# Kernel tuning notes

Hardware: AMD Instinct MI355X
Metric: run time of the kernel (lower is better)

Reference implementation:

```python
import jax, jax.numpy as jnp
import numpy as np

B, S, D, H, RANK, NC = 2, 2048, 1024, 16, 128, 16
DH = D // H


def setup_inputs() -> dict:
    key = jax.random.key(0)
    ks = jax.random.split(key, 10)
    x = jax.random.normal(ks[0], (B, S, D), jnp.float32)
    # causal mask, broadcast over batch and heads like torch's [B,1,S,S]
    mask = jnp.tril(jnp.ones((S, S), dtype=bool))[None, None]
    # orthogonal-ish init approximated by scaled gaussian
    compress_neurons = jax.random.normal(ks[1], (NC, D, RANK), jnp.float32) / np.sqrt(D)
    router_Q = jax.random.normal(ks[2], (NC, D), jnp.float32) * 0.02
    router_K = jax.random.normal(ks[3], (NC, D), jnp.float32) * 0.02
    router_V = jax.random.normal(ks[4], (NC, D), jnp.float32) * 0.02
    wQ = jax.random.normal(ks[5], (D, RANK), jnp.float32) / np.sqrt(RANK)
    wK = jax.random.normal(ks[6], (D, RANK), jnp.float32) / np.sqrt(RANK)
    wV = jax.random.normal(ks[7], (D, RANK), jnp.float32) / np.sqrt(RANK)
    wO = jax.random.normal(ks[8], (D, D), jnp.float32) / np.sqrt(D)
    return {"x": x, "mask": mask, "compress_neurons": compress_neurons,
            "router_Q": router_Q, "router_K": router_K, "router_V": router_V,
            "wQ": wQ, "wK": wK, "wV": wV, "wO": wO}


def reference(x, mask, compress_neurons, router_Q, router_K, router_V, wQ, wK, wV, wO):
    def compress(router_w):
        # router scores -> softmax over all n_compress neurons
        w = jax.nn.softmax(jnp.einsum('bsd,nd->bsn', x, router_w), axis=-1)  # [B,S,NC]
        # softmax-weighted sum of all neuron projections (fused einsum)
        return jnp.einsum('bsd,ndr,bsn->bsr', x, compress_neurons, w)  # [B,S,RANK]

    hQ = compress(router_Q)
    hK = compress(router_K)
    hV = compress(router_V)
    # expand rank -> d_model (Linear weight [D,RANK]), then split heads
    Q = jnp.einsum('bsr,dr->bsd', hQ, wQ).reshape(B, S, H, DH).transpose(0, 2, 1, 3)
    K = jnp.einsum('bsr,dr->bsd', hK, wK).reshape(B, S, H, DH).transpose(0, 2, 1, 3)
    V = jnp.einsum('bsr,dr->bsd', hV, wV).reshape(B, S, H, DH).transpose(0, 2, 1, 3)
    scores = jnp.einsum('bhqd,bhkd->bhqk', Q, K) / np.sqrt(DH)  # [B,H,S,S]
    scores = jnp.where(mask, scores, -jnp.inf)
    attn = jax.nn.softmax(scores, axis=-1)
    attn_out = jnp.einsum('bhqk,bhkd->bhqd', attn, V)
    attn_out = attn_out.transpose(0, 2, 1, 3).reshape(B, S, D)
    # dropout omitted (eval mode / dropout=0)
    return jnp.einsum('bsd,ed->bse', attn_out, wO)
```

## Files before the change

kernel.cpp:

```cpp
#include <hip/hip_runtime.h>
#include <hip/hip_bf16.h>
#include <math.h>

#define B_ 2
#define S_ 2048
#define D_ 1024
#define H_ 16
#define RANK_ 128
#define NC_ 16
#define DH_ 64
#define T_ (B_*S_)
#define NZ_ 2176

typedef __attribute__((ext_vector_type(8))) __bf16 bf16x8;
typedef __attribute__((ext_vector_type(8))) unsigned short u16x8;
typedef __attribute__((ext_vector_type(4))) float f32x4;

#if __has_builtin(__builtin_amdgcn_exp2f)
#define EXP2F(x) __builtin_amdgcn_exp2f(x)
#else
#define EXP2F(x) exp2f(x)
#endif

__device__ __forceinline__ unsigned short f2bu(float f) {
    __hip_bfloat16 h = __float2bfloat16(f);
    unsigned short u; __builtin_memcpy(&u, &h, 2); return u;
}
__device__ __forceinline__ float bu2f(unsigned short u) {
    __hip_bfloat16 h; __builtin_memcpy(&h, &u, 2); return __bfloat162float(h);
}

__device__ __forceinline__ void gl_lds16(const unsigned short* g, unsigned short* l) {
    __builtin_amdgcn_global_load_lds(
        (const __attribute__((address_space(1))) void*)g,
        (__attribute__((address_space(3))) void*)l, 16, 0, 0);
}

__device__ __forceinline__ bool sniff_f32(const unsigned* __restrict__ p) {
    int votes = 0;
    #pragma unroll
    for (int i = 0; i < 64; i++) {
        unsigned e = (p[i] >> 23) & 0xFFu;
        votes += (e >= 0x60u && e <= 0x8Fu) ? 1 : 0;
    }
    return votes >= 32;
}

struct Cvt { const void* src[9]; unsigned short* dst[9]; const void* C; unsigned short* Ct; };

__global__ __launch_bounds__(256) void k_inputs(Cvt cv,
    const unsigned* __restrict__ probe)
{
    bool f32 = sniff_f32(probe);
    if (blockIdx.x < 512) {
        int bid = blockIdx.x;
        int d0 = (bid & 15) * 64, r0 = ((bid >> 4) & 1) * 64, n = bid >> 5;
        __shared__ unsigned short tile[64][65];
        for (int idx = threadIdx.x; idx < 4096; idx += 256) {
            int row = idx >> 6, col = idx & 63;
            size_t si = ((size_t)n*D_ + d0 + row)*RANK_ + r0 + col;
            tile[row][col] = f32 ? f2bu(((const float*)cv.C)[si])
                                 : ((const unsigned short*)cv.C)[si];
        }
        __syncthreads();
        for (int idx = threadIdx.x; idx < 4096; idx += 256) {
            int row = idx >> 6, col = idx & 63;
            cv.Ct[((size_t)(n*RANK_ + r0 + row))*D_ + d0 + col] = tile[col][row];
        }
        return;
    }
    const int offs[9] = {0, 4194304, 4210688, 4227072, 4243456,
                         4259840, 4390912, 4521984, 4653056};
    const int total = 5701632;
    int nconv = gridDim.x - 512;
    int stride = nconv * 256;
    for (int i = (blockIdx.x - 512) * 256 + threadIdx.x; i < total; i += stride) {
        int seg = 0;
        #pragma unroll
        for (int s = 1; s < 9; s++) seg += (i >= offs[s]) ? 1 : 0;
        int local = i - offs[seg];
        const void* sp = cv.src[seg];
        unsigned short v = 0;
        if (sp) v = f32 ? f2bu(((const float*)sp)[local]) : ((const unsigned short*)sp)[local];
        cv.dst[seg][local] = v;
    }
}

__global__ __launch_bounds__(256) void k_transposeV(const unsigned short* __restrict__ V,
    unsigned short* __restrict__ Vtg)
{
    int t0 = blockIdx.x * 64, hcol = blockIdx.y;
    __shared__ unsigned short tile[64][65];
    for (int idx = threadIdx.x; idx < 4096; idx += 256) {
        int row = idx >> 6, col = idx & 63;
        tile[row][col] = V[(size_t)(t0 + row)*D_ + hcol*64 + col];
    }
    __syncthreads();
    int bb = t0 >> 11, s0 = t0 & 2047;
    for (int idx = threadIdx.x; idx < 4096; idx += 256) {
        int dh = idx >> 6, col = idx & 63;
        Vtg[(size_t)((bb*H_ + hcol)*64 + dh)*S_ + s0 + col] = tile[col][dh];
    }
}

template<int MT, int MODE>
__global__ __launch_bounds__(256) void k_mfma_gemm(const unsigned short* __restrict__ A0,
    const unsigned short* __restrict__ Bm, void* __restrict__ Cout,
    const unsigned* __restrict__ probe, int M, int N, int K)
{
    bool f32out = false;
    if (MODE == 2) f32out = sniff_f32(probe);
    __shared__ __align__(16) unsigned short As[MT*32*32];
    __shared__ __align__(16) unsigned short Bs[128*32];
    const int tid = threadIdx.x;
    const int wv = tid >> 6, lane = tid & 63;
    const int wm = (wv >> 1) * (MT*16), wn = (wv & 1) * 64;
    const int quad = lane >> 4, l16 = lane & 15;
    const int m0 = blockIdx.x * (MT*32), n0 = blockIdx.y * 128;

    const unsigned short* A = A0;
    unsigned short* outb = (unsigned short*)Cout;
    int colBase = n0, outStride = N;
    float scale = 1.f;
    if (MODE == 1) {
        int w = n0 >> 10;
        A = A0 + (size_t)w * T_ * RANK_;
        outb = (unsigned short*)Cout + (size_t)w * T_ * D_;
        colBase = n0 & 1023; outStride = D_;
        if (w == 0) scale = 0.125f * 1.44269504f;
    }

    const f32x4 z4 = {0.f, 0.f, 0.f, 0.f};
    f32x4 acc[MT][4];
    #pragma unroll
    for (int i = 0; i < MT; i++)
        #pragma unroll
        for (int j = 0; j < 4; j++) acc[i][j] = z4;

    for (int k0 = 0; k0 < K; k0 += 32) {
        __syncthreads();
        #pragma unroll
        for (int c = 0; c < MT/2; c++) {
            int idx = wv*64 + c*256 + lane;
            gl_lds16(A + (size_t)(m0 + (idx >> 2))*K + k0 + (idx & 3)*8,
                     &As[(wv*64 + c*256)*8]);
        }
        #pragma unroll
        for (int c = 0; c < 2; c++) {
            int idx = wv*64 + c*256 + lane;
            gl_lds16(Bm + (size_t)(n0 + (idx >> 2))*K + k0 + (idx & 3)*8,
                     &Bs[(wv*64 + c*256)*8]);
        }
        __syncthreads();
        bf16x8 af[MT], bfr[4];
        #pragma unroll
        for (int mt = 0; mt < MT; mt++) af[mt]  = *(const bf16x8*)&As[(wm + mt*16 + l16)*32 + quad*8];
        #pragma unroll
        for (int nt = 0; nt < 4; nt++) bfr[nt] = *(const bf16x8*)&Bs[(wn + nt*16 + l16)*32 + quad*8];
        #pragma unroll
        for (int mt = 0; mt < MT; mt++)
            #pragma unroll
            for (int nt = 0; nt < 4; nt++)
                acc[mt][nt] = __builtin_amdgcn_mfma_f32_16x16x32_bf16(af[mt], bfr[nt], acc[mt][nt], 0, 0, 0);
    }
    #pragma unroll
    for (int mt = 0; mt < MT; mt++)
        #pragma unroll
        for (int nt = 0; nt < 4; nt++) {
            int col = colBase + wn + nt*16 + l16;
            #pragma unroll
            for (int r = 0; r < 4; r++) {
                int rowg = m0 + wm + mt*16 + quad*4 + r;
                float v = acc[mt][nt][r] * scale;
                if (MODE == 2 && f32out) ((float*)Cout)[(size_t)rowg*outStride + col] = v;
                else                     outb[(size_t)rowg*outStride + col] = f2bu(v);
            }
        }
}

__global__ __launch_bounds__(256) void k_hreduce(const unsigned short* __restrict__ z,
    unsigned short* __restrict__ h)
{
    int t0 = blockIdx.x * 2;
    int tg = threadIdx.x >> 7, r = threadIdx.x & 127;
    int t = t0 + tg;
    __shared__ float sc[2][48];
    __shared__ float wl[2][3][16];
    if (threadIdx.x < 96) {
        int tk = threadIdx.x / 48, j = threadIdx.x % 48;
        sc[tk][j] = bu2f(z[(size_t)(t0 + tk)*NZ_ + 2048 + j]);
    }
    __syncthreads();
    if (threadIdx.x < 6) {
        int tk = threadIdx.x / 3, w = threadIdx.x % 3;
        float m = -INFINITY;
        for (int n = 0; n < 16; n++) m = fmaxf(m, sc[tk][w*16 + n]);
        float s = 0.f, e[16];
        for (int n = 0; n < 16; n++) { e[n] = __expf(sc[tk][w*16 + n] - m); s += e[n]; }
        float inv = 1.f / s;
        for (int n = 0; n < 16; n++) wl[tk][w][n] = e[n] * inv;
    }
    __syncthreads();
    const unsigned short* zr = z + (size_t)t * NZ_;
    float acc[3] = {0.f, 0.f, 0.f};
    #pragma unroll
    for (int n = 0; n < NC_; n++) {
        float zv = bu2f(zr[n*RANK_ + r]);
        #pragma unroll
        for (int w = 0; w < 3; w++) acc[w] += wl[tg][w][n] * zv;
    }
    #pragma unroll
    for (int w = 0; w < 3; w++) h[((size_t)w*T_ + t)*RANK_ + r] = f2bu(acc[w]);
}

__global__ __launch_bounds__(256) void k_flash_mfma(const unsigned short* __restrict__ Qm,
    const unsigned short* __restrict__ Km, const unsigned short* __restrict__ Vtg,
    unsigned short* __restrict__ Om)
{
    const int p = blockIdx.x, hh = blockIdx.y, b = blockIdx.z;
    __shared__ __align__(16) unsigned short Ks[128*64];
    __shared__ __align__(16) unsigned short Vt[64*128];
    __shared__ __align__(16) unsigned short Ps[64][136];
    const int tid = threadIdx.x;
    const int w = tid >> 6, lane = tid & 63;
    const int quad = lane >> 4, l16 = lane & 15;
    const size_t base  = ((size_t)b * S_) * D_ + (size_t)hh * DH_;
    const size_t vbase = (size_t)((b*H_ + hh) * 64) * S_;
    const f32x4 z4 = {0.f, 0.f, 0.f, 0.f};

    for (int rep = 0; rep < 2; rep++) {
        const int qt = rep ? (31 - p) : p;

        bf16x8 aq[2];
        #pragma unroll
        for (int s = 0; s < 2; s++)
            aq[s] = *(const bf16x8*)(Qm + base + (size_t)(qt*64 + w*16 + l16)*D_ + s*32 + quad*8);

        f32x4 oacc[4];
        #pragma unroll
        for (int nt = 0; nt < 4; nt++) oacc[nt] = z4;
        float lsum[4] = {0.f, 0.f, 0.f, 0.f};

        const int nkt = (qt >> 1) + 1;
        for (int kt = 0; kt < nkt; kt++) {
            __syncthreads();
            #pragma unroll
            for (int c = 0; c < 4; c++) {
                int idx = c*256 + tid;
                int row = idx >> 3, j = (idx & 7) ^ (row & 7);
                gl_lds16(Km + base + (size_t)(kt*128 + row)*D_ + j*8, &Ks[(c*256 + (w<<6))*8]);
            }
            #pragma unroll
            for (int c = 0; c < 4; c++) {
                int idx = c*256 + tid;
                int row = idx >> 4, j = (idx & 15) ^ (row & 7);
                gl_lds16(Vtg + vbase + (size_t)row*S_ + kt*128 + j*8, &Vt[(c*256 + (w<<6))*8]);
            }
            __syncthreads();

            f32x4 sacc[8];
            #pragma unroll
            for (int nt = 0; nt < 8; nt++) sacc[nt] = z4;
            #pragma unroll
            for (int s = 0; s < 2; s++)
                #pragma unroll
                for (int nt = 0; nt < 8; nt++) {
                    int row = nt*16 + l16;
                    int cc = (s*4 + quad) ^ (row & 7);
                    bf16x8 bk = *(const bf16x8*)&Ks[row*64 + cc*8];
                    sacc[nt] = __builtin_amdgcn_mfma_f32_16x16x32_bf16(aq[s], bk, sacc[nt], 0, 0, 0);
                }
            if (kt == (qt >> 1)) {
                #pragma unroll
                for (int nt = 0; nt < 8; nt++) {
                    int key = kt*128 + nt*16 + l16;
                    #pragma unroll
                    for (int r = 0; r < 4; r++)
                        if (key > qt*64 + w*16 + quad*4 + r) sacc[nt][r] = -INFINITY;
                }
            }
            #pragma unroll
            for (int r = 0; r < 4; r++) {
                float rs = 0.f;
                #pragma unroll
                for (int nt = 0; nt < 8; nt++) {
                    float pv = EXP2F(sacc[nt][r]);
                    rs += pv;
                    Ps[w*16 + quad*4 + r][nt*16 + l16] = f2bu(pv);
                }
                lsum[r] += rs;
            }
            #pragma unroll
            for (int s = 0; s < 4; s++) {
                bf16x8 ap = *(const bf16x8*)&Ps[w*16 + l16][s*32 + quad*8];
                #pragma unroll
                for (int nt = 0; nt < 4; nt++) {
                    int row = nt*16 + l16;
                    int cc = (s*4 + quad) ^ (row & 7);
                    bf16x8 bv = *(const bf16x8*)&Vt[row*128 + cc*8];
                    oacc[nt] = __builtin_amdgcn_mfma_f32_16x16x32_bf16(ap, bv, oacc[nt], 0, 0, 0);
                }
            }
        }
        #pragma unroll
        for (int r = 0; r < 4; r++) {
            float l = lsum[r];
            #pragma unroll
            for (int off = 1; off < 16; off <<= 1) l += __shfl_xor(l, off, 64);
            float inv = 1.f / l;
            int tok = qt*64 + w*16 + quad*4 + r;
            #pragma unroll
            for (int nt = 0; nt < 4; nt++)
                Om[base + (size_t)tok*D_ + nt*16 + l16] = f2bu(oacc[nt][r] * inv);
        }
    }
}

extern "C" void kernel_launch(void* const* d_in, const int* in_sizes, int n_in,
                              void* d_out, int out_size, void* d_ws, size_t ws_size,
                              hipStream_t stream)
{
    const unsigned* probe = (const unsigned*)d_in[0];

    unsigned short* u = (unsigned short*)d_ws;
    unsigned short* xc   = u;               size_t o = (size_t)T_*D_;
    unsigned short* wqkv = u + o;           o += (size_t)3*D_*RANK_;
    unsigned short* wOc  = u + o;           o += (size_t)D_*D_;
    unsigned short* Ct   = u + o;           o += (size_t)NZ_*D_;
    unsigned short* h3   = u + o;           o += (size_t)3*T_*RANK_;
    unsigned short* QKVb = u + o;           o += (size_t)3*T_*D_;
    unsigned short* Vtg  = u + o;           o += (size_t)T_*D_;
    unsigned short* z    = u + o;           o += (size_t)T_*NZ_;
    unsigned short* attnb= u + o;           o += (size_t)T_*D_;

    unsigned short* Rp = Ct + (size_t)2048*D_;
    unsigned short* Qb = QKVb;
    unsigned short* Kb = QKVb + (size_t)T_*D_;
    unsigned short* Vb = QKVb + (size_t)2*T_*D_;

    Cvt cv;
    cv.src[0] = d_in[0]; cv.dst[0] = xc;
    cv.src[1] = d_in[3]; cv.dst[1] = Rp;
    cv.src[2] = d_in[4]; cv.dst[2] = Rp + 16384;
    cv.src[3] = d_in[5]; cv.dst[3] = Rp + 32768;
    cv.src[4] = nullptr; cv.dst[4] = Rp + 49152;
    cv.src[5] = d_in[6]; cv.dst[5] = wqkv;
    cv.src[6] = d_in[7]; cv.dst[6] = wqkv + 131072;
    cv.src[7] = d_in[8]; cv.dst[7] = wqkv + 262144;
    cv.src[8] = d_in[9]; cv.dst[8] = wOc;
    cv.C = d_in[2]; cv.Ct = Ct;
    k_inputs<<<512 + 2048, 256, 0, stream>>>(cv, probe);

    k_mfma_gemm<4,0><<<dim3(T_/128, NZ_/128), 256, 0, stream>>>(
        xc, Ct, z, nullptr, T_, NZ_, D_);

    k_hreduce<<<T_/2, 256, 0, stream>>>(z, h3);

    k_mfma_gemm<4,1><<<dim3(T_/128, 3*D_/128), 256, 0, stream>>>(
        h3, wqkv, QKVb, nullptr, T_, 3*D_, RANK_);

    k_transposeV<<<dim3(T_/64, H_), 256, 0, stream>>>(Vb, Vtg);

    k_flash_mfma<<<dim3(16, H_, B_), 256, 0, stream>>>(Qb, Kb, Vtg, attnb);

    k_mfma_gemm<2,2><<<dim3(T_/64, D_/128), 256, 0, stream>>>(
        attnb, wOc, d_out, probe, T_, D_, D_);
}
```

Before: 245.8 us.

## Fuse V transpose into QKV GEMM and double-buffer K tiles in flash attention

A new QKV kernel computes Q and K as before and computes V transposed directly by swapping GEMM operands, which removes the separate transpose kernel and one full write and read of V. The flash attention kernel now double-buffers K tiles in LDS, prefetching the next tile while computing on the current one. V fragments are loaded straight from global memory into registers instead of being staged through LDS. This removes a kernel launch and a sync per iteration, but raises register pressure, and the direct V loads in the flash loop are strided rather than coalesced.

```diff
diff --git a/kernel.cpp b/kernel.cpp
--- a/kernel.cpp
+++ b/kernel.cpp
@@ -86,25 +86,8 @@
     }
 }
 
-__global__ __launch_bounds__(256) void k_transposeV(const unsigned short* __restrict__ V,
-    unsigned short* __restrict__ Vtg)
-{
-    int t0 = blockIdx.x * 64, hcol = blockIdx.y;
-    __shared__ unsigned short tile[64][65];
-    for (int idx = threadIdx.x; idx < 4096; idx += 256) {
-        int row = idx >> 6, col = idx & 63;
-        tile[row][col] = V[(size_t)(t0 + row)*D_ + hcol*64 + col];
-    }
-    __syncthreads();
-    int bb = t0 >> 11, s0 = t0 & 2047;
-    for (int idx = threadIdx.x; idx < 4096; idx += 256) {
-        int dh = idx >> 6, col = idx & 63;
-        Vtg[(size_t)((bb*H_ + hcol)*64 + dh)*S_ + s0 + col] = tile[col][dh];
-    }
-}
-
 template<int MT, int MODE>
-__global__ __launch_bounds__(256) void k_mfma_gemm(const unsigned short* __restrict__ A0,
+__global__ __launch_bounds__(256) void k_mfma_gemm(const unsigned short* __restrict__ A,
     const unsigned short* __restrict__ Bm, void* __restrict__ Cout,
     const unsigned* __restrict__ probe, int M, int N, int K)
 {
@@ -118,18 +101,6 @@
     const int quad = lane >> 4, l16 = lane & 15;
     const int m0 = blockIdx.x * (MT*32), n0 = blockIdx.y * 128;
 
-    const unsigned short* A = A0;
-    unsigned short* outb = (unsigned short*)Cout;
-    int colBase = n0, outStride = N;
-    float scale = 1.f;
-    if (MODE == 1) {
-        int w = n0 >> 10;
-        A = A0 + (size_t)w * T_ * RANK_;
-        outb = (unsigned short*)Cout + (size_t)w * T_ * D_;
-        colBase = n0 & 1023; outStride = D_;
-        if (w == 0) scale = 0.125f * 1.44269504f;
-    }
-
     const f32x4 z4 = {0.f, 0.f, 0.f, 0.f};
     f32x4 acc[MT][4];
     #pragma unroll
@@ -167,13 +138,93 @@
     for (int mt = 0; mt < MT; mt++)
         #pragma unroll
         for (int nt = 0; nt < 4; nt++) {
-            int col = colBase + wn + nt*16 + l16;
+            int col = n0 + wn + nt*16 + l16;
             #pragma unroll
             for (int r = 0; r < 4; r++) {
                 int rowg = m0 + wm + mt*16 + quad*4 + r;
+                float v = acc[mt][nt][r];
+                if (MODE == 2 && f32out) ((float*)Cout)[(size_t)rowg*N + col] = v;
+                else  ((unsigned short*)Cout)[(size_t)rowg*N + col] = f2bu(v);
+            }
+        }
+}
+
+__global__ __launch_bounds__(256) void k_qkv2(const unsigned short* __restrict__ h3,
+    const unsigned short* __restrict__ wqkv, unsigned short* __restrict__ QKb,
+    unsigned short* __restrict__ Vtg)
+{
+    __shared__ __align__(16) unsigned short As[128*32];
+    __shared__ __align__(16) unsigned short Bs[128*32];
+    const int tid = threadIdx.x;
+    const int wv = tid >> 6, lane = tid & 63;
+    const int wm = (wv >> 1) * 64, wn = (wv & 1) * 64;
+    const int quad = lane >> 4, l16 = lane & 15;
+
+    const bool vt = (blockIdx.x >= 512);
+    int m0, n0;
+    const unsigned short *A, *Bm;
+    float scale = 1.f;
+    if (!vt) {
+        int id = blockIdx.x;
+        m0 = (id & 31) * 128;
+        n0 = (id >> 5) * 128;
+        int w = n0 >> 10;
+        A  = h3 + (size_t)w * T_ * RANK_ + (size_t)m0 * RANK_;
+        Bm = wqkv + (size_t)w * D_ * RANK_ + (size_t)(n0 & 1023) * RANK_;
+        if (w == 0) scale = 0.125f * 1.44269504f;
+    } else {
+        int id = blockIdx.x - 512;
+        m0 = (id & 7) * 128;
+        n0 = (id >> 3) * 128;
+        A  = wqkv + (size_t)2 * D_ * RANK_ + (size_t)m0 * RANK_;
+        Bm = h3 + (size_t)2 * T_ * RANK_ + (size_t)n0 * RANK_;
+    }
+
+    const f32x4 z4 = {0.f, 0.f, 0.f, 0.f};
+    f32x4 acc[4][4];
+    #pragma unroll
+    for (int i = 0; i < 4; i++)
+        #pragma unroll
+        for (int j = 0; j < 4; j++) acc[i][j] = z4;
+
+    for (int k0 = 0; k0 < RANK_; k0 += 32) {
+        __syncthreads();
+        #pragma unroll
+        for (int c = 0; c < 2; c++) {
+            int idx = wv*64 + c*256 + lane;
+            gl_lds16(A  + (size_t)(idx >> 2)*RANK_ + k0 + (idx & 3)*8,
+                     &As[(wv*64 + c*256)*8]);
+            gl_lds16(Bm + (size_t)(idx >> 2)*RANK_ + k0 + (idx & 3)*8,
+                     &Bs[(wv*64 + c*256)*8]);
+        }
+        __syncthreads();
+        bf16x8 af[4], bfr[4];
+        #pragma unroll
+        for (int mt = 0; mt < 4; mt++) af[mt]  = *(const bf16x8*)&As[(wm + mt*16 + l16)*32 + quad*8];
+        #pragma unroll
+        for (int nt = 0; nt < 4; nt++) bfr[nt] = *(const bf16x8*)&Bs[(wn + nt*16 + l16)*32 + quad*8];
+        #pragma unroll
+        for (int mt = 0; mt < 4; mt++)
+            #pragma unroll
+            for (int nt = 0; nt < 4; nt++)
+                acc[mt][nt] = __builtin_amdgcn_mfma_f32_16x16x32_bf16(af[mt], bfr[nt], acc[mt][nt], 0, 0, 0);
+    }
+    #pragma unroll
+    for (int mt = 0; mt < 4; mt++)
+        #pragma unroll
+        for (int nt = 0; nt < 4; nt++) {
+            #pragma unroll
+            for (int r = 0; r < 4; r++) {
+                int rowg = m0 + wm + mt*16 + quad*4 + r;
+                int col  = n0 + wn + nt*16 + l16;
                 float v = acc[mt][nt][r] * scale;
-                if (MODE == 2 && f32out) ((float*)Cout)[(size_t)rowg*outStride + col] = v;
-                else                     outb[(size_t)rowg*outStride + col] = f2bu(v);
+                if (!vt) {
+                    QKb[(size_t)(col >> 10)*T_*D_ + (size_t)rowg*D_ + (col & 1023)]
+                        = f2bu(v);
+                } else {
+                    size_t vrow = (size_t)((col >> 11)*H_ + (rowg >> 6))*64 + (rowg & 63);
+                    Vtg[vrow*S_ + (col & 2047)] = f2bu(v);
+                }
             }
         }
 }
@@ -218,8 +269,7 @@
     unsigned short* __restrict__ Om)
 {
     const int p = blockIdx.x, hh = blockIdx.y, b = blockIdx.z;
-    __shared__ __align__(16) unsigned short Ks[128*64];
-    __shared__ __align__(16) unsigned short Vt[64*128];
+    __shared__ __align__(16) unsigned short Ks[2][128*64];
     __shared__ __align__(16) unsigned short Ps[64][136];
     const int tid = threadIdx.x;
     const int w = tid >> 6, lane = tid & 63;
@@ -242,21 +292,35 @@
         float lsum[4] = {0.f, 0.f, 0.f, 0.f};
 
         const int nkt = (qt >> 1) + 1;
+
+        __syncthreads();
+        #pragma unroll
+        for (int c = 0; c < 4; c++) {
+            int idx = c*256 + tid;
+            int row = idx >> 3, j = (idx & 7) ^ (row & 7);
+            gl_lds16(Km + base + (size_t)row*D_ + j*8, &Ks[0][(c*256 + (w<<6))*8]);
+        }
+
         for (int kt = 0; kt < nkt; kt++) {
+            const int cur = kt & 1;
             __syncthreads();
-            #pragma unroll
-            for (int c = 0; c < 4; c++) {
-                int idx = c*256 + tid;
-                int row = idx >> 3, j = (idx & 7) ^ (row & 7);
-                gl_lds16(Km + base + (size_t)(kt*128 + row)*D_ + j*8, &Ks[(c*256 + (w<<6))*8]);
-            }
-            #pragma unroll
-            for (int c = 0; c < 4; c++) {
-                int idx = c*256 + tid;
-                int row = idx >> 4, j = (idx & 15) ^ (row & 7);
-                gl_lds16(Vtg + vbase + (size_t)row*S_ + kt*128 + j*8, &Vt[(c*256 + (w<<6))*8]);
-            }
-            __syncthreads();
+
+            bf16x8 vf[4][4];
+            #pragma unroll
+            for (int s = 0; s < 4; s++)
+                #pragma unroll
+                for (int nt = 0; nt < 4; nt++)
+                    vf[s][nt] = *(const bf16x8*)(Vtg + vbase + (size_t)(nt*16 + l16)*S_
+                                                 + kt*128 + s*32 + quad*8);
+            if (kt + 1 < nkt) {
+                #pragma unroll
+                for (int c = 0; c < 4; c++) {
+                    int idx = c*256 + tid;
+                    int row = idx >> 3, j = (idx & 7) ^ (row & 7);
+                    gl_lds16(Km + base + (size_t)((kt+1)*128 + row)*D_ + j*8,
+                             &Ks[1-cur][(c*256 + (w<<6))*8]);
+                }
+            }
 
             f32x4 sacc[8];
             #pragma unroll
@@ -267,7 +331,7 @@
                 for (int nt = 0; nt < 8; nt++) {
                     int row = nt*16 + l16;
                     int cc = (s*4 + quad) ^ (row & 7);
-                    bf16x8 bk = *(const bf16x8*)&Ks[row*64 + cc*8];
+                    bf16x8 bk = *(const bf16x8*)&Ks[cur][row*64 + cc*8];
                     sacc[nt] = __builtin_amdgcn_mfma_f32_16x16x32_bf16(aq[s], bk, sacc[nt], 0, 0, 0);
                 }
             if (kt == (qt >> 1)) {
@@ -294,12 +358,8 @@
             for (int s = 0; s < 4; s++) {
                 bf16x8 ap = *(const bf16x8*)&Ps[w*16 + l16][s*32 + quad*8];
                 #pragma unroll
-                for (int nt = 0; nt < 4; nt++) {
-                    int row = nt*16 + l16;
-                    int cc = (s*4 + quad) ^ (row & 7);
-                    bf16x8 bv = *(const bf16x8*)&Vt[row*128 + cc*8];
-                    oacc[nt] = __builtin_amdgcn_mfma_f32_16x16x32_bf16(ap, bv, oacc[nt], 0, 0, 0);
-                }
+                for (int nt = 0; nt < 4; nt++)
+                    oacc[nt] = __builtin_amdgcn_mfma_f32_16x16x32_bf16(ap, vf[s][nt], oacc[nt], 0, 0, 0);
             }
         }
         #pragma unroll
@@ -328,15 +388,14 @@
     unsigned short* wOc  = u + o;           o += (size_t)D_*D_;
     unsigned short* Ct   = u + o;           o += (size_t)NZ_*D_;
     unsigned short* h3   = u + o;           o += (size_t)3*T_*RANK_;
-    unsigned short* QKVb = u + o;           o += (size_t)3*T_*D_;
+    unsigned short* QKb  = u + o;           o += (size_t)2*T_*D_;
     unsigned short* Vtg  = u + o;           o += (size_t)T_*D_;
     unsigned short* z    = u + o;           o += (size_t)T_*NZ_;
     unsigned short* attnb= u + o;           o += (size_t)T_*D_;
 
     unsigned short* Rp = Ct + (size_t)2048*D_;
-    unsigned short* Qb = QKVb;
-    unsigned short* Kb = QKVb + (size_t)T_*D_;
-    unsigned short* Vb = QKVb + (size_t)2*T_*D_;
+    unsigned short* Qb = QKb;
+    unsigned short* Kb = QKb + (size_t)T_*D_;
 
     Cvt cv;
     cv.src[0] = d_in[0]; cv.dst[0] = xc;
@@ -356,10 +415,7 @@
 
     k_hreduce<<<T_/2, 256, 0, stream>>>(z, h3);
 
-    k_mfma_gemm<4,1><<<dim3(T_/128, 3*D_/128), 256, 0, stream>>>(
-        h3, wqkv, QKVb, nullptr, T_, 3*D_, RANK_);
-
-    k_transposeV<<<dim3(T_/64, H_), 256, 0, stream>>>(Vb, Vtg);
+    k_qkv2<<<768, 256, 0, stream>>>(h3, wqkv, QKb, Vtg);
 
     k_flash_mfma<<<dim3(16, H_, B_), 256, 0, stream>>>(Qb, Kb, Vtg, attnb);
 
```

Measured after the change: 268.9 us. 1.09x slower.
